# Optimization experiments

Hardware: AMD Instinct MI355X
Metric: run time of the kernel (lower is better)

The kernel has to match this reference:

```python
import jax, jax.numpy as jnp
import numpy as np

B, S, DIM = 32, 1, 4096
NH, NKV, HD = 32, 8, 128
N_REP = NH // NKV
MAX_SEQ = 2048
START_POS = 2047


def setup_inputs() -> dict:
    key = jax.random.key(0)
    ks = jax.random.split(key, 10)
    t = jnp.arange(S) + START_POS  # absolute positions of the new tokens
    inv_freq = 1.0 / (10000.0 ** (jnp.arange(0, HD, 2, dtype=jnp.float32) / HD))  # [HD/2]
    angles = t[:, None].astype(jnp.float32) * inv_freq[None, :]  # [S, HD/2]
    return {
        "x": jax.random.normal(ks[0], (B, S, DIM), dtype=jnp.float32),
        "freqs_cos": jnp.cos(angles),
        "freqs_sin": jnp.sin(angles),
        "cache_k": jax.random.normal(ks[1], (B, MAX_SEQ, NKV, HD), dtype=jnp.float32),
        "cache_v": jax.random.normal(ks[2], (B, MAX_SEQ, NKV, HD), dtype=jnp.float32),
        "wq": jax.random.normal(ks[3], (NH * HD, DIM), dtype=jnp.float32) * 0.02,
        "wk": jax.random.normal(ks[4], (NKV * HD, DIM), dtype=jnp.float32) * 0.02,
        "wv": jax.random.normal(ks[5], (NKV * HD, DIM), dtype=jnp.float32) * 0.02,
        "wo": jax.random.normal(ks[6], (NH * HD, DIM), dtype=jnp.float32).T * 0.02,  # stored [out,in]=[DIM, NH*HD]
        "start_pos": START_POS,
    }


def _apply_rope(t, cos, sin):
    # t: [B, S, H, HD]; cos/sin: [S, HD/2] -> broadcast [1, S, 1, HD/2]
    tr = t.reshape(*t.shape[:-1], HD // 2, 2)
    x0, x1 = tr[..., 0], tr[..., 1]
    c = cos[None, :, None, :]
    s = sin[None, :, None, :]
    o0 = x0 * c - x1 * s
    o1 = x0 * s + x1 * c
    return jnp.stack([o0, o1], axis=-1).reshape(t.shape)


def reference(x, freqs_cos, freqs_sin, cache_k, cache_v, wq, wk, wv, wo, start_pos):
    batch, seq_len, _ = x.shape
    xq = jnp.einsum('bsd,ed->bse', x, wq).reshape(batch, seq_len, NH, HD)
    xk = jnp.einsum('bsd,ed->bse', x, wk).reshape(batch, seq_len, NKV, HD)
    xv = jnp.einsum('bsd,ed->bse', x, wv).reshape(batch, seq_len, NKV, HD)

    xq = _apply_rope(xq, freqs_cos, freqs_sin)
    xk = _apply_rope(xk, freqs_cos, freqs_sin)

    # KV-cache scatter-write, then read prefix [0, start_pos+seq_len)
    ck = jax.lax.dynamic_update_slice(cache_k, xk, (0, start_pos, 0, 0))
    cv = jax.lax.dynamic_update_slice(cache_v, xv, (0, start_pos, 0, 0))
    T = start_pos + seq_len  # static Python int
    keys = ck[:, :T]    # [B, T, NKV, HD]
    values = cv[:, :T]  # [B, T, NKV, HD]

    # GQA without materializing repeat_kv: group query heads by kv head
    q = xq.reshape(batch, seq_len, NKV, N_REP, HD)
    scores = jnp.einsum('bsgrd,btgd->bgrst', q, keys) / jnp.sqrt(jnp.float32(HD))
    probs = jax.nn.softmax(scores.astype(jnp.float32), axis=-1).astype(xq.dtype)
    out = jnp.einsum('bgrst,btgd->bsgrd', probs, values)  # [B, S, NKV, N_REP, HD]
    out = out.reshape(batch, seq_len, NH * HD)
    return jnp.einsum('bse,de->bsd', out, wo)
```

## Files before the change

kernel.cpp:

```cpp
#include <hip/hip_runtime.h>
#include <hip/hip_bf16.h>

#define B     32
#define DIM   4096
#define NH    32
#define NKV   8
#define HD    128
#define TCACHE 2048
#define NREP  4
#define SPLIT 8
#define TS    256
#define CHUNK 256
#define NCH   (DIM / CHUNK)

__device__ __forceinline__ void gemm16_core(
    const float* __restrict__ inp, const float* __restrict__ W,
    float* __restrict__ outp, int stride, int row0, bool rope,
    const float* __restrict__ fc, const float* __restrict__ fs,
    float (*xs)[B][CHUNK])
{
    const int tid = threadIdx.x;
    const int rp  = tid >> 6;
    const int kt  = tid & 63;
    const int r0  = row0 + rp * 2;

    const float* w0 = W + (size_t)r0 * DIM;
    const float* w1 = w0 + DIM;

    const int sb = tid >> 4;
    const int sc = (tid << 4) & 255;
    const float* sbase = inp + (size_t)sb * DIM + sc;

    float acc0[B], acc1[B];
#pragma unroll
    for (int b = 0; b < B; ++b) { acc0[b] = 0.f; acc1[b] = 0.f; }

    float4 xr0 = *(const float4*)(sbase);
    float4 xr1 = *(const float4*)(sbase + 4);
    float4 xr2 = *(const float4*)(sbase + 8);
    float4 xr3 = *(const float4*)(sbase + 12);
    float4 wa0 = *(const float4*)(w0 + kt * 4);
    float4 wa1 = *(const float4*)(w1 + kt * 4);
    *(float4*)(&xs[0][sb][sc])      = xr0;
    *(float4*)(&xs[0][sb][sc + 4])  = xr1;
    *(float4*)(&xs[0][sb][sc + 8])  = xr2;
    *(float4*)(&xs[0][sb][sc + 12]) = xr3;

    int buf = 0;
    for (int ch = 0; ch < NCH; ++ch) {
        __syncthreads();
        float4 wb0, wb1;
        const bool more = (ch + 1 < NCH);
        if (more) {
            const int k1 = (ch + 1) * CHUNK;
            xr0 = *(const float4*)(sbase + k1);
            xr1 = *(const float4*)(sbase + k1 + 4);
            xr2 = *(const float4*)(sbase + k1 + 8);
            xr3 = *(const float4*)(sbase + k1 + 12);
            wb0 = *(const float4*)(w0 + k1 + kt * 4);
            wb1 = *(const float4*)(w1 + k1 + kt * 4);
        }
        const float* xrow = &xs[buf][0][kt * 4];
#pragma unroll
        for (int b = 0; b < B; ++b) {
            float4 xv = *(const float4*)(xrow + b * CHUNK);
            acc0[b] = fmaf(wa0.x, xv.x, acc0[b]);
            acc0[b] = fmaf(wa0.y, xv.y, acc0[b]);
            acc0[b] = fmaf(wa0.z, xv.z, acc0[b]);
            acc0[b] = fmaf(wa0.w, xv.w, acc0[b]);
            acc1[b] = fmaf(wa1.x, xv.x, acc1[b]);
            acc1[b] = fmaf(wa1.y, xv.y, acc1[b]);
            acc1[b] = fmaf(wa1.z, xv.z, acc1[b]);
            acc1[b] = fmaf(wa1.w, xv.w, acc1[b]);
        }
        if (more) {
            *(float4*)(&xs[buf ^ 1][sb][sc])      = xr0;
            *(float4*)(&xs[buf ^ 1][sb][sc + 4])  = xr1;
            *(float4*)(&xs[buf ^ 1][sb][sc + 8])  = xr2;
            *(float4*)(&xs[buf ^ 1][sb][sc + 12]) = xr3;
            wa0 = wb0; wa1 = wb1;
        }
        buf ^= 1;
    }

#pragma unroll
    for (int b = 0; b < B; ++b) {
        float v0 = acc0[b], v1 = acc1[b];
        for (int off = 1; off < 64; off <<= 1) {
            v0 += __shfl_xor(v0, off);
            v1 += __shfl_xor(v1, off);
        }
        acc0[b] = v0; acc1[b] = v1;
    }
    if (kt == 0) {
        float c = 1.f, s = 0.f;
        if (rope) { int i = (r0 & (HD - 1)) >> 1; c = fc[i]; s = fs[i]; }
#pragma unroll
        for (int b = 0; b < B; ++b) {
            float o0 = acc0[b], o1 = acc1[b];
            if (rope) { float t0 = o0 * c - o1 * s; o1 = o0 * s + o1 * c; o0 = t0; }
            outp[(size_t)b * stride + r0]     = o0;
            outp[(size_t)b * stride + r0 + 1] = o1;
        }
    }
}

__global__ __launch_bounds__(512) void qkv_gemm(
    const float* __restrict__ x,
    const float* __restrict__ wq, const float* __restrict__ wk, const float* __restrict__ wv,
    float* __restrict__ qo, float* __restrict__ ko, float* __restrict__ vo,
    const float* __restrict__ fc, const float* __restrict__ fs)
{
    __shared__ float xs[2][B][CHUNK];
    int blk = blockIdx.x;
    const float* W; float* outp; int stride, row0; bool rope;
    if (blk < 256)      { W = wq; outp = qo; stride = NH * HD;  row0 = blk * 16;         rope = true;  }
    else if (blk < 320) { W = wk; outp = ko; stride = NKV * HD; row0 = (blk - 256) * 16; rope = true;  }
    else                { W = wv; outp = vo; stride = NKV * HD; row0 = (blk - 320) * 16; rope = false; }
    gemm16_core(x, W, outp, stride, row0, rope, fc, fs, xs);
}

__global__ __launch_bounds__(512) void gemm_wo(
    const float* __restrict__ inp, const float* __restrict__ W, float* __restrict__ outp)
{
    __shared__ float xs[2][B][CHUNK];
    gemm16_core(inp, W, outp, DIM, blockIdx.x * 16, false, nullptr, nullptr, xs);
}

__global__ __launch_bounds__(256) void attn_split_k(
    const float* __restrict__ qr, const float* __restrict__ kn, const float* __restrict__ vn,
    const float* __restrict__ ck, const float* __restrict__ cv,
    float* __restrict__ part_o, float* __restrict__ part_ml)
{
    __shared__ float q_lds[NREP][HD];
    __shared__ float p_lds[TS][NREP];
    __shared__ float red[4][NREP];
    __shared__ float o_scr[8][NREP][HD];

    const int bid = blockIdx.x;
    const int s = bid & 7, h = (bid >> 3) & 7, b = bid >> 6;
    const int t0 = s * TS;
    const int tid = threadIdx.x;

    for (int i = tid; i < NREP * HD; i += 256)
        q_lds[i >> 7][i & 127] = qr[((size_t)b * NH + h * NREP + (i >> 7)) * HD + (i & 127)];
    __syncthreads();

    const int t = t0 + tid;
    const float* kptr = (t == TCACHE - 1)
        ? (kn + ((size_t)b * NKV + h) * HD)
        : (ck + (((size_t)b * TCACHE + t) * NKV + h) * HD);
    float s0 = 0.f, s1 = 0.f, s2 = 0.f, s3 = 0.f;
#pragma unroll 8
    for (int d = 0; d < HD; d += 4) {
        float4 kv = *(const float4*)(kptr + d);
        float4 q0 = *(const float4*)(&q_lds[0][d]);
        float4 q1 = *(const float4*)(&q_lds[1][d]);
        float4 q2 = *(const float4*)(&q_lds[2][d]);
        float4 q3 = *(const float4*)(&q_lds[3][d]);
        s0 = fmaf(q0.x, kv.x, s0); s0 = fmaf(q0.y, kv.y, s0); s0 = fmaf(q0.z, kv.z, s0); s0 = fmaf(q0.w, kv.w, s0);
        s1 = fmaf(q1.x, kv.x, s1); s1 = fmaf(q1.y, kv.y, s1); s1 = fmaf(q1.z, kv.z, s1); s1 = fmaf(q1.w, kv.w, s1);
        s2 = fmaf(q2.x, kv.x, s2); s2 = fmaf(q2.y, kv.y, s2); s2 = fmaf(q2.z, kv.z, s2); s2 = fmaf(q2.w, kv.w, s2);
        s3 = fmaf(q3.x, kv.x, s3); s3 = fmaf(q3.y, kv.y, s3); s3 = fmaf(q3.z, kv.z, s3); s3 = fmaf(q3.w, kv.w, s3);
    }
    const float scale = 0.088388347648318447f;
    s0 *= scale; s1 *= scale; s2 *= scale; s3 *= scale;

    float m0 = s0, m1 = s1, m2 = s2, m3 = s3;
    for (int off = 1; off < 64; off <<= 1) {
        m0 = fmaxf(m0, __shfl_xor(m0, off));
        m1 = fmaxf(m1, __shfl_xor(m1, off));
        m2 = fmaxf(m2, __shfl_xor(m2, off));
        m3 = fmaxf(m3, __shfl_xor(m3, off));
    }
    const int wv_ = tid >> 6, lane = tid & 63;
    if (lane == 0) { red[wv_][0] = m0; red[wv_][1] = m1; red[wv_][2] = m2; red[wv_][3] = m3; }
    __syncthreads();
    m0 = fmaxf(fmaxf(red[0][0], red[1][0]), fmaxf(red[2][0], red[3][0]));
    m1 = fmaxf(fmaxf(red[0][1], red[1][1]), fmaxf(red[2][1], red[3][1]));
    m2 = fmaxf(fmaxf(red[0][2], red[1][2]), fmaxf(red[2][2], red[3][2]));
    m3 = fmaxf(fmaxf(red[0][3], red[1][3]), fmaxf(red[2][3], red[3][3]));
    float p0 = __expf(s0 - m0), p1 = __expf(s1 - m1), p2 = __expf(s2 - m2), p3 = __expf(s3 - m3);
    *(float4*)(&p_lds[tid][0]) = make_float4(p0, p1, p2, p3);
    float l0 = p0, l1 = p1, l2 = p2, l3 = p3;
    for (int off = 1; off < 64; off <<= 1) {
        l0 += __shfl_xor(l0, off);
        l1 += __shfl_xor(l1, off);
        l2 += __shfl_xor(l2, off);
        l3 += __shfl_xor(l3, off);
    }
    __syncthreads();
    if (lane == 0) { red[wv_][0] = l0; red[wv_][1] = l1; red[wv_][2] = l2; red[wv_][3] = l3; }
    __syncthreads();
    if (tid < NREP) {
        float l = red[0][tid] + red[1][tid] + red[2][tid] + red[3][tid];
        float m = (tid == 0) ? m0 : (tid == 1) ? m1 : (tid == 2) ? m2 : m3;
        part_ml[(size_t)bid * 8 + tid * 2]     = m;
        part_ml[(size_t)bid * 8 + tid * 2 + 1] = l;
    }

    const int g  = tid >> 5;
    const int dl = (tid & 31) << 2;
    float4 a0 = make_float4(0,0,0,0), a1 = a0, a2 = a0, a3 = a0;
    const int tb = t0 + g * 32;
#pragma unroll 4
    for (int j = 0; j < 32; ++j) {
        int tt = tb + j;
        const float* vptr = (tt == TCACHE - 1)
            ? (vn + ((size_t)b * NKV + h) * HD)
            : (cv + (((size_t)b * TCACHE + tt) * NKV + h) * HD);
        float4 vvv = *(const float4*)(vptr + dl);
        float4 pp  = *(const float4*)(&p_lds[g * 32 + j][0]);
        a0.x = fmaf(pp.x, vvv.x, a0.x); a0.y = fmaf(pp.x, vvv.y, a0.y); a0.z = fmaf(pp.x, vvv.z, a0.z); a0.w = fmaf(pp.x, vvv.w, a0.w);
        a1.x = fmaf(pp.y, vvv.x, a1.x); a1.y = fmaf(pp.y, vvv.y, a1.y); a1.z = fmaf(pp.y, vvv.z, a1.z); a1.w = fmaf(pp.y, vvv.w, a1.w);
        a2.x = fmaf(pp.z, vvv.x, a2.x); a2.y = fmaf(pp.z, vvv.y, a2.y); a2.z = fmaf(pp.z, vvv.z, a2.z); a2.w = fmaf(pp.z, vvv.w, a2.w);
        a3.x = fmaf(pp.w, vvv.x, a3.x); a3.y = fmaf(pp.w, vvv.y, a3.y); a3.z = fmaf(pp.w, vvv.z, a3.z); a3.w = fmaf(pp.w, vvv.w, a3.w);
    }
    *(float4*)(&o_scr[g][0][dl]) = a0;
    *(float4*)(&o_scr[g][1][dl]) = a1;
    *(float4*)(&o_scr[g][2][dl]) = a2;
    *(float4*)(&o_scr[g][3][dl]) = a3;
    __syncthreads();
    for (int oi = tid; oi < NREP * HD; oi += 256) {
        int r = oi >> 7, d = oi & 127;
        float sum = 0.f;
#pragma unroll
        for (int gg = 0; gg < 8; ++gg) sum += o_scr[gg][r][d];
        part_o[((size_t)bid * NREP + r) * HD + d] = sum;
    }
}

__global__ __launch_bounds__(128) void attn_combine(
    const float* __restrict__ part_o, const float* __restrict__ part_ml,
    float* __restrict__ attn_out)
{
    const int bh = blockIdx.x;
    const int d  = threadIdx.x;
    const int b = bh >> 3, h = bh & 7;
#pragma unroll
    for (int r = 0; r < NREP; ++r) {
        float ms[SPLIT], ls[SPLIT];
        float M = -1e30f;
#pragma unroll
        for (int s = 0; s < SPLIT; ++s) {
            ms[s] = part_ml[(size_t)(bh * SPLIT + s) * 8 + r * 2];
            ls[s] = part_ml[(size_t)(bh * SPLIT + s) * 8 + r * 2 + 1];
            M = fmaxf(M, ms[s]);
        }
        float L = 0.f, o = 0.f;
#pragma unroll
        for (int s = 0; s < SPLIT; ++s) {
            float w = __expf(ms[s] - M);
            L += ls[s] * w;
            o = fmaf(w, part_o[((size_t)(bh * SPLIT + s) * NREP + r) * HD + d], o);
        }
        attn_out[((size_t)b * NH + (h * NREP + r)) * HD + d] = o / L;
    }
}

extern "C" void kernel_launch(void* const* d_in, const int* in_sizes, int n_in,
                              void* d_out, int out_size, void* d_ws, size_t ws_size,
                              hipStream_t stream)
{
    const float* x  = (const float*)d_in[0];
    const float* fc = (const float*)d_in[1];
    const float* fs = (const float*)d_in[2];
    const float* ck = (const float*)d_in[3];
    const float* cv = (const float*)d_in[4];
    const float* wq = (const float*)d_in[5];
    const float* wk = (const float*)d_in[6];
    const float* wv = (const float*)d_in[7];
    const float* wo = (const float*)d_in[8];

    float* ws   = (float*)d_ws;
    float* q_r  = ws;
    float* k_n  = ws + 131072;
    float* v_n  = ws + 163840;
    float* a_o  = ws + 196608;
    float* p_o  = ws + 327680;
    float* p_ml = ws + 1376256;
    float* outp = (float*)d_out;

    qkv_gemm<<<dim3(384), dim3(512), 0, stream>>>(x, wq, wk, wv, q_r, k_n, v_n, fc, fs);
    attn_split_k<<<dim3(B * NKV * SPLIT), dim3(256), 0, stream>>>(q_r, k_n, v_n, ck, cv, p_o, p_ml);
    attn_combine<<<dim3(B * NKV), dim3(128), 0, stream>>>(p_o, p_ml, a_o);
    gemm_wo<<<dim3(256), dim3(512), 0, stream>>>(a_o, wo, outp);
}
```

Baseline: 214.2 us.

## Retile GEMV core to 4 rows by 16 batches per wave with distributed epilogue

Each wave of the projection GEMM now computes 4 weight rows for half the batch, where before it computed 2 rows for the full batch. Each LDS x-vector load is therefore reused across 4 weight rows instead of 2. The final reduction hands each lane one output, and RoPE is applied by exchanging partner values through a shuffle, so stores are spread across lanes instead of coming from lane 0 alone. Launch bounds now request 2 blocks per CU, which risks register spills with 64 accumulators per thread, and the shuffle reduction count stays at 64 values per wave.

```diff
diff --git a/kernel.cpp b/kernel.cpp
--- a/kernel.cpp
+++ b/kernel.cpp
@@ -11,101 +11,104 @@
 #define SPLIT 8
 #define TS    256
 #define CHUNK 256
-#define NCH   (DIM / CHUNK)
-
-__device__ __forceinline__ void gemm16_core(
+
+__device__ __forceinline__ void gemm_core_v3(
     const float* __restrict__ inp, const float* __restrict__ W,
     float* __restrict__ outp, int stride, int row0, bool rope,
     const float* __restrict__ fc, const float* __restrict__ fs,
     float (*xs)[B][CHUNK])
 {
     const int tid = threadIdx.x;
-    const int rp  = tid >> 6;
+    const int wid = tid >> 6;
     const int kt  = tid & 63;
-    const int r0  = row0 + rp * 2;
-
-    const float* w0 = W + (size_t)r0 * DIM;
-    const float* w1 = w0 + DIM;
+    const int rg  = wid >> 1;
+    const int bh  = wid & 1;
+    const int r0  = row0 + rg * 4;
+    const int b0  = bh * 16;
+
+    const float* wp = W + (size_t)r0 * DIM;
 
     const int sb = tid >> 4;
-    const int sc = (tid << 4) & 255;
+    const int sc = (tid & 15) * 16;
     const float* sbase = inp + (size_t)sb * DIM + sc;
 
-    float acc0[B], acc1[B];
-#pragma unroll
-    for (int b = 0; b < B; ++b) { acc0[b] = 0.f; acc1[b] = 0.f; }
-
-    float4 xr0 = *(const float4*)(sbase);
-    float4 xr1 = *(const float4*)(sbase + 4);
-    float4 xr2 = *(const float4*)(sbase + 8);
-    float4 xr3 = *(const float4*)(sbase + 12);
-    float4 wa0 = *(const float4*)(w0 + kt * 4);
-    float4 wa1 = *(const float4*)(w1 + kt * 4);
-    *(float4*)(&xs[0][sb][sc])      = xr0;
-    *(float4*)(&xs[0][sb][sc + 4])  = xr1;
-    *(float4*)(&xs[0][sb][sc + 8])  = xr2;
-    *(float4*)(&xs[0][sb][sc + 12]) = xr3;
+    float acc[4][16];
+#pragma unroll
+    for (int r = 0; r < 4; ++r)
+#pragma unroll
+        for (int b = 0; b < 16; ++b) acc[r][b] = 0.f;
+
+    float4 xr[4], wa[4];
+#pragma unroll
+    for (int j = 0; j < 4; ++j) xr[j] = *(const float4*)(sbase + j * 4);
+#pragma unroll
+    for (int r = 0; r < 4; ++r) wa[r] = *(const float4*)(wp + (size_t)r * DIM + kt * 4);
+#pragma unroll
+    for (int j = 0; j < 4; ++j)
+        *(float4*)(&xs[0][sb][sc + j * 4]) = xr[j];
 
     int buf = 0;
-    for (int ch = 0; ch < NCH; ++ch) {
+    for (int ch = 0; ch < DIM / CHUNK; ++ch) {
         __syncthreads();
-        float4 wb0, wb1;
-        const bool more = (ch + 1 < NCH);
+        const bool more = (ch + 1 < DIM / CHUNK);
+        float4 wb[4];
         if (more) {
             const int k1 = (ch + 1) * CHUNK;
-            xr0 = *(const float4*)(sbase + k1);
-            xr1 = *(const float4*)(sbase + k1 + 4);
-            xr2 = *(const float4*)(sbase + k1 + 8);
-            xr3 = *(const float4*)(sbase + k1 + 12);
-            wb0 = *(const float4*)(w0 + k1 + kt * 4);
-            wb1 = *(const float4*)(w1 + k1 + kt * 4);
-        }
-        const float* xrow = &xs[buf][0][kt * 4];
-#pragma unroll
-        for (int b = 0; b < B; ++b) {
+#pragma unroll
+            for (int j = 0; j < 4; ++j) xr[j] = *(const float4*)(sbase + k1 + j * 4);
+#pragma unroll
+            for (int r = 0; r < 4; ++r) wb[r] = *(const float4*)(wp + k1 + (size_t)r * DIM + kt * 4);
+        }
+        const float* xrow = &xs[buf][b0][kt * 4];
+#pragma unroll
+        for (int b = 0; b < 16; ++b) {
             float4 xv = *(const float4*)(xrow + b * CHUNK);
-            acc0[b] = fmaf(wa0.x, xv.x, acc0[b]);
-            acc0[b] = fmaf(wa0.y, xv.y, acc0[b]);
-            acc0[b] = fmaf(wa0.z, xv.z, acc0[b]);
-            acc0[b] = fmaf(wa0.w, xv.w, acc0[b]);
-            acc1[b] = fmaf(wa1.x, xv.x, acc1[b]);
-            acc1[b] = fmaf(wa1.y, xv.y, acc1[b]);
-            acc1[b] = fmaf(wa1.z, xv.z, acc1[b]);
-            acc1[b] = fmaf(wa1.w, xv.w, acc1[b]);
+#pragma unroll
+            for (int r = 0; r < 4; ++r) {
+                acc[r][b] = fmaf(wa[r].x, xv.x, acc[r][b]);
+                acc[r][b] = fmaf(wa[r].y, xv.y, acc[r][b]);
+                acc[r][b] = fmaf(wa[r].z, xv.z, acc[r][b]);
+                acc[r][b] = fmaf(wa[r].w, xv.w, acc[r][b]);
+            }
         }
         if (more) {
-            *(float4*)(&xs[buf ^ 1][sb][sc])      = xr0;
-            *(float4*)(&xs[buf ^ 1][sb][sc + 4])  = xr1;
-            *(float4*)(&xs[buf ^ 1][sb][sc + 8])  = xr2;
-            *(float4*)(&xs[buf ^ 1][sb][sc + 12]) = xr3;
-            wa0 = wb0; wa1 = wb1;
+#pragma unroll
+            for (int j = 0; j < 4; ++j)
+                *(float4*)(&xs[buf ^ 1][sb][sc + j * 4]) = xr[j];
+#pragma unroll
+            for (int r = 0; r < 4; ++r) wa[r] = wb[r];
         }
         buf ^= 1;
     }
 
-#pragma unroll
-    for (int b = 0; b < B; ++b) {
-        float v0 = acc0[b], v1 = acc1[b];
-        for (int off = 1; off < 64; off <<= 1) {
-            v0 += __shfl_xor(v0, off);
-            v1 += __shfl_xor(v1, off);
-        }
-        acc0[b] = v0; acc1[b] = v1;
-    }
-    if (kt == 0) {
-        float c = 1.f, s = 0.f;
-        if (rope) { int i = (r0 & (HD - 1)) >> 1; c = fc[i]; s = fs[i]; }
-#pragma unroll
-        for (int b = 0; b < B; ++b) {
-            float o0 = acc0[b], o1 = acc1[b];
-            if (rope) { float t0 = o0 * c - o1 * s; o1 = o0 * s + o1 * c; o0 = t0; }
-            outp[(size_t)b * stride + r0]     = o0;
-            outp[(size_t)b * stride + r0 + 1] = o1;
-        }
-    }
-}
-
-__global__ __launch_bounds__(512) void qkv_gemm(
+    float myout = 0.f;
+#pragma unroll
+    for (int r = 0; r < 4; ++r) {
+#pragma unroll
+        for (int bb = 0; bb < 16; ++bb) {
+            float v = acc[r][bb];
+#pragma unroll
+            for (int off = 1; off < 64; off <<= 1) v += __shfl_xor(v, off);
+            if (kt == r * 16 + bb) myout = v;
+        }
+    }
+
+    const int orow = kt >> 4;
+    const int ob   = b0 + (kt & 15);
+    float res;
+    if (rope) {
+        const float prt = __shfl_xor(myout, 16);
+        const int gr = r0 + orow;
+        const int fi = (gr & (HD - 1)) >> 1;
+        const float c = fc[fi], s = fs[fi];
+        res = (gr & 1) ? fmaf(myout, c, prt * s) : fmaf(myout, c, -prt * s);
+    } else {
+        res = myout;
+    }
+    outp[(size_t)ob * stride + r0 + orow] = res;
+}
+
+__global__ __launch_bounds__(512, 2) void qkv_gemm(
     const float* __restrict__ x,
     const float* __restrict__ wq, const float* __restrict__ wk, const float* __restrict__ wv,
     float* __restrict__ qo, float* __restrict__ ko, float* __restrict__ vo,
@@ -117,14 +120,14 @@
     if (blk < 256)      { W = wq; outp = qo; stride = NH * HD;  row0 = blk * 16;         rope = true;  }
     else if (blk < 320) { W = wk; outp = ko; stride = NKV * HD; row0 = (blk - 256) * 16; rope = true;  }
     else                { W = wv; outp = vo; stride = NKV * HD; row0 = (blk - 320) * 16; rope = false; }
-    gemm16_core(x, W, outp, stride, row0, rope, fc, fs, xs);
-}
-
-__global__ __launch_bounds__(512) void gemm_wo(
+    gemm_core_v3(x, W, outp, stride, row0, rope, fc, fs, xs);
+}
+
+__global__ __launch_bounds__(512, 2) void gemm_wo(
     const float* __restrict__ inp, const float* __restrict__ W, float* __restrict__ outp)
 {
     __shared__ float xs[2][B][CHUNK];
-    gemm16_core(inp, W, outp, DIM, blockIdx.x * 16, false, nullptr, nullptr, xs);
+    gemm_core_v3(inp, W, outp, DIM, blockIdx.x * 16, false, nullptr, nullptr, xs);
 }
 
 __global__ __launch_bounds__(256) void attn_split_k(
```

Result: no change. 211.2 us (-1.4%).
